# Optimization experiments

Measured on AMD Instinct MI355X. Metric: run time of the kernel, lower is better.

## Reference

```python
import jax, jax.numpy as jnp
import numpy as np

B, D_INPUT, D_MODEL, MEM, HID, N_SYNCH, OUT_DIMS, ITERS = 128, 512, 2048, 25, 32, 256, 1000, 24
SYNC = N_SYNCH * (N_SYNCH + 1) // 2  # 32896


def setup_inputs() -> dict:
    key = jax.random.key(0)
    ks = jax.random.split(key, 12)
    inp = {
        'x': jax.random.normal(ks[0], (B, D_INPUT), jnp.float32),
        'syn_w': jax.random.normal(ks[1], (D_INPUT + D_MODEL, 2 * D_MODEL), jnp.float32) * 0.02,
        'syn_b': jnp.zeros((2 * D_MODEL,), jnp.float32),
        'ln_g': jnp.ones((D_MODEL,), jnp.float32),
        'ln_b': jnp.zeros((D_MODEL,), jnp.float32),
        'tp_w1': jax.random.normal(ks[2], (MEM, 2 * HID, D_MODEL), jnp.float32) * (1.0 / np.sqrt(MEM + 2 * HID)),
        'tp_b1': jnp.zeros((1, D_MODEL, 2 * HID), jnp.float32),
        'tp_w2': jax.random.normal(ks[3], (HID, 2, D_MODEL), jnp.float32) * (1.0 / np.sqrt(HID + 2)),
        'tp_b2': jnp.zeros((1, D_MODEL, 2), jnp.float32),
        'start_activated_state': jax.random.normal(ks[4], (D_MODEL,), jnp.float32) * (1.0 / np.sqrt(D_MODEL)),
        'start_trace': jax.random.normal(ks[5], (D_MODEL, MEM), jnp.float32) * (1.0 / np.sqrt(D_MODEL + MEM)),
        'decay_params_out': jax.random.uniform(ks[6], (SYNC,), jnp.float32),
        'out_w': jax.random.normal(ks[7], (SYNC, OUT_DIMS), jnp.float32) * 0.02,
        'out_b': jnp.zeros((OUT_DIMS,), jnp.float32),
        'idx_left': jax.random.randint(ks[8], (N_SYNCH,), 0, D_MODEL),
        'idx_right': jax.random.randint(ks[9], (N_SYNCH,), 0, D_MODEL),
        'iterations': ITERS,
    }
    return inp


def _glu(z):
    a, b = jnp.split(z, 2, axis=-1)
    return a * jax.nn.sigmoid(b)


def reference(x, syn_w, syn_b, ln_g, ln_b, tp_w1, tp_b1, tp_w2, tp_b2,
              start_activated_state, start_trace, decay_params_out, out_w, out_b,
              idx_left, idx_right, iterations):
    Bx = x.shape[0]
    D, M = start_trace.shape
    n_synch = idx_left.shape[0]
    iu, ju = np.triu_indices(n_synch)
    r = jnp.exp(-jnp.clip(decay_params_out, 0.0, 15.0))[None, :]  # (1, S)
    log_nc = np.log(out_b.shape[0]).astype(np.float32)

    def pairwise(act):  # act: (B, D) -> (B, S) upper-tri of outer product of selected neurons
        l = act[:, idx_left]
        rr = act[:, idx_right]
        outer = l[:, :, None] * rr[:, None, :]
        return outer[:, iu, ju]

    def trace_proc(trace):  # (B, D, M) -> (B, D) per-neuron MLP (NLM)
        h = _glu(jnp.einsum('BDM,MHD->BDH', trace, tp_w1) + tp_b1)
        o = _glu(jnp.einsum('BDH,HOD->BDO', h, tp_w2) + tp_b2)
        return o[..., 0]

    def layernorm(z):
        mu = jnp.mean(z, -1, keepdims=True)
        var = jnp.mean((z - mu) ** 2, -1, keepdims=True)
        return (z - mu) * jax.lax.rsqrt(var + 1e-5) * ln_g + ln_b

    act0 = jnp.broadcast_to(start_activated_state[None, :], (Bx, D))
    trace0 = jnp.broadcast_to(start_trace[None, :, :], (Bx, D, M))
    alpha0 = pairwise(act0)
    beta0 = jnp.ones_like(alpha0)

    def step(carry, _):
        trace, act, alpha, beta = carry
        pre = jnp.concatenate([x, act], axis=-1)
        state = layernorm(_glu(pre @ syn_w + syn_b))            # (B, D)
        trace = jnp.concatenate([trace[:, :, 1:], state[:, :, None]], axis=-1)
        act = trace_proc(trace)                                  # (B, D)
        pp = pairwise(act)
        alpha = r * alpha + pp
        beta = r * beta + 1.0
        sync = alpha / jnp.sqrt(beta)                            # (B, S)
        pred = sync @ out_w + out_b                              # (B, out)
        logp = jax.nn.log_softmax(pred, axis=-1)
        ne = -jnp.sum(jnp.exp(logp) * logp, axis=-1) / log_nc
        cert = jnp.stack([ne, 1.0 - ne], axis=-1)                # (B, 2)
        return (trace, act, alpha, beta), (pred, cert)

    _, (preds, certs) = jax.lax.scan(step, (trace0, act0, alpha0, beta0), None, length=iterations)
    predictions = jnp.moveaxis(preds, 0, -1)   # (B, out_dims, T)
    certainties = jnp.moveaxis(certs, 0, -1)   # (B, 2, T)
    return predictions, certainties
```

## Files before the change

### kernel.cpp

```cpp
#include <hip/hip_runtime.h>
#include <stdint.h>

#define BB      128
#define DIN     512
#define DMODEL  2048
#define MEMN    25
#define NSY     256
#define OUTD    1000
#define ITERS   24
#define SYNCN   32896
#define KPAD    33792
#define NPAD    1024
#define NSPLIT  32
#define KCH     1056
#define PREDTOT (BB*OUTD*ITERS)

typedef __attribute__((ext_vector_type(8))) short bf16x8;
typedef __attribute__((ext_vector_type(4))) float f32x4;

__device__ __forceinline__ unsigned short f2bf(float x){
    unsigned int u = __float_as_uint(x);
    u += 0x7fffu + ((u >> 16) & 1u);
    return (unsigned short)(u >> 16);
}
__device__ __forceinline__ float bf2f(unsigned short h){
    unsigned int u = ((unsigned int)h) << 16;
    return __uint_as_float(u);
}
__device__ __forceinline__ float sigm(float x){ return 1.f/(1.f + __expf(-x)); }

__device__ __forceinline__ void gload16(const unsigned short* g, unsigned short* l){
    __builtin_amdgcn_global_load_lds(
        (const __attribute__((address_space(1))) unsigned int*)(const void*)g,
        (__attribute__((address_space(3))) unsigned int*)(void*)l,
        16, 0, 0);
}

__device__ __forceinline__ void reduce_row(const float* __restrict__ part, const float* __restrict__ outb,
    float* __restrict__ dout, float* red, int b, int t, int tid){
    float v[4];
    float m = -1e30f;
#pragma unroll
    for (int q = 0; q < 4; ++q){
        int n = q*256 + tid;
        float s;
        if (n < OUTD){
            s = outb[n];
            for (int sk = 0; sk < NSPLIT; ++sk)
                s += part[(long)sk*(BB*NPAD) + (long)b*NPAD + n];
        } else s = -1e30f;
        v[q] = s;
        m = fmaxf(m, s);
    }
#pragma unroll
    for (int off = 32; off; off >>= 1) m = fmaxf(m, __shfl_down(m, off));
    int w = tid >> 6;
    if ((tid & 63) == 0) red[w] = m;
    __syncthreads();
    float M = fmaxf(fmaxf(red[0], red[1]), fmaxf(red[2], red[3]));
    __syncthreads();
    float z = 0.f, s2 = 0.f;
#pragma unroll
    for (int q = 0; q < 4; ++q){
        int n = q*256 + tid;
        if (n < OUTD){
            float e = __expf(v[q] - M);
            z += e; s2 += e*v[q];
        }
    }
#pragma unroll
    for (int off = 32; off; off >>= 1){
        z  += __shfl_down(z, off);
        s2 += __shfl_down(s2, off);
    }
    if ((tid & 63) == 0){ red[w] = z; red[4+w] = s2; }
    __syncthreads();
    if (tid == 0){
        float Z = red[0]+red[1]+red[2]+red[3];
        float S = red[4]+red[5]+red[6]+red[7];
        float logZ = M + __logf(Z);
        float ne = (logZ - S/Z) / 6.907755278982137f;
        dout[PREDTOT + b*48 + t] = ne;
        dout[PREDTOT + b*48 + 24 + t] = 1.f - ne;
    }
#pragma unroll
    for (int q = 0; q < 4; ++q){
        int n = q*256 + tid;
        if (n < OUTD) dout[(long)b*(OUTD*ITERS) + (long)n*ITERS + t] = v[q];
    }
}


__global__ __launch_bounds__(256) void init_trace_k(const float* __restrict__ st,
    unsigned short* __restrict__ trh, unsigned short* __restrict__ trl){
    const long N = (long)MEMN*DMODEL*BB;
    for (long i = (long)blockIdx.x*256 + threadIdx.x; i < N; i += (long)gridDim.x*256){
        int m = (int)(i / (DMODEL*BB));
        int rem = (int)(i % (DMODEL*BB));
        int d = rem >> 7;
        float v = st[d*MEMN + m];
        unsigned short h = f2bf(v);
        trh[i] = h;
        trl[i] = f2bf(v - bf2f(h));
    }
}

__global__ __launch_bounds__(256) void init_act_k(const float* __restrict__ sas, float* __restrict__ act){
    for (int i = blockIdx.x*256 + threadIdx.x; i < DMODEL*BB; i += gridDim.x*256)
        act[i] = sas[i >> 7];
}

__global__ __launch_bounds__(256) void init_alpha_k(const float* __restrict__ sas,
    const int* __restrict__ il, const int* __restrict__ ir, float* __restrict__ alpha){
    int i = blockIdx.x, tid = threadIdx.x;
    if (tid >= NSY - i) return;
    int j = i + tid;
    int k = i*(2*NSY - i + 1)/2 + tid;
    float a0 = sas[il[i]] * sas[ir[j]];
    for (int b = 0; b < BB; ++b) alpha[b*SYNCN + k] = a0;
}

__global__ __launch_bounds__(256) void init_rowmap_k(int* __restrict__ rowOf, int* __restrict__ rowstart){
    int i = blockIdx.x, tid = threadIdx.x;
    int start = i*(2*NSY - i + 1)/2;
    int len = NSY - i;
    if (tid == 0) rowstart[i] = start;
    for (int t = tid; t < len; t += 256) rowOf[start + t] = i;
}

__global__ __launch_bounds__(256) void transpose_f32_k(const float* __restrict__ in, float* __restrict__ out, int R, int C){
    __shared__ float S[64][65];
    int r0 = blockIdx.y*64, c0 = blockIdx.x*64;
    for (int i = threadIdx.x; i < 64*64; i += 256){
        int rr = i >> 6, cc = i & 63;
        int r = r0+rr, c = c0+cc;
        if (r < R && c < C) S[rr][cc] = in[(long)r*C + c];
    }
    __syncthreads();
    for (int i = threadIdx.x; i < 64*64; i += 256){
        int cc = i >> 6, rr = i & 63;
        int r = r0+rr, c = c0+cc;
        if (r < R && c < C) out[(long)c*R + r] = S[rr][cc];
    }
}

__global__ __launch_bounds__(256) void w1bf_prep_k(const float* __restrict__ w1t, unsigned short* __restrict__ w1bf){
    int d = blockIdx.x, tid = threadIdx.x;
    __shared__ float S[1600];
    for (int i = tid; i < 1600; i += 256) S[i] = w1t[(long)d*1600 + i];
    __syncthreads();
    for (int i = tid; i < 2048; i += 256){
        int h = i >> 5, m = i & 31;
        float v = (m < MEMN) ? S[m*64 + h] : 0.f;
        unsigned short hi = f2bf(v);
        unsigned short lo = f2bf(v - bf2f(hi));
        w1bf[(long)d*4096 + i]        = hi;
        w1bf[(long)d*4096 + 2048 + i] = lo;
    }
}

__global__ __launch_bounds__(256) void wbf_transpose_k(const float* __restrict__ w, unsigned short* __restrict__ wt){
    __shared__ float S[64][65];
    int k0 = blockIdx.x*64, n0 = blockIdx.y*64;
    int tid = threadIdx.x;
    if (k0 >= SYNCN){
        uint4 z = {0u,0u,0u,0u};
#pragma unroll
        for (int p = 0; p < 2; ++p){
            int i = tid + p*256;
            int nn = i >> 3, k8 = (i & 7)*8;
            *(uint4*)(wt + (long)(n0+nn)*KPAD + k0 + k8) = z;
        }
        return;
    }
    const long MAXI = (long)SYNCN*OUTD - 4;
#pragma unroll
    for (int p = 0; p < 4; ++p){
        int i = tid + p*256;
        int rr = i >> 4, c4 = (i & 15)*4;
        long idx = (long)(k0+rr)*OUTD + n0 + c4;
        if (idx > MAXI) idx = MAXI;
        float4 v = *(const float4*)(w + idx);
        S[rr][c4+0]=v.x; S[rr][c4+1]=v.y; S[rr][c4+2]=v.z; S[rr][c4+3]=v.w;
    }
    __syncthreads();
#pragma unroll
    for (int p = 0; p < 4; ++p){
        int i = tid + p*256;
        int nn = i >> 4, k4 = (i & 15)*4;
        ushort4 o;
        o.x = f2bf(S[k4+0][nn]); o.y = f2bf(S[k4+1][nn]);
        o.z = f2bf(S[k4+2][nn]); o.w = f2bf(S[k4+3][nn]);
        *(ushort4*)(wt + (long)(n0+nn)*KPAD + k0 + k4) = o;
    }
}

__global__ __launch_bounds__(256) void swt_convert_k(const float* __restrict__ w,
    unsigned short* __restrict__ th, unsigned short* __restrict__ tl){
    __shared__ float S[64][65];
    int k0 = blockIdx.x*64, n0 = blockIdx.y*64;
    int tid = threadIdx.x;
#pragma unroll
    for (int p = 0; p < 4; ++p){
        int i = tid + p*256;
        int rr = i >> 4, c4 = (i & 15)*4;
        float4 v = *(const float4*)(w + (long)(512 + k0 + rr)*4096 + n0 + c4);
        S[rr][c4+0]=v.x; S[rr][c4+1]=v.y; S[rr][c4+2]=v.z; S[rr][c4+3]=v.w;
    }
    __syncthreads();
#pragma unroll
    for (int p = 0; p < 4; ++p){
        int i = tid + p*256;
        int nn = i >> 4, k4 = (i & 15)*4;
        ushort4 oh, ol;
        float v0 = S[k4+0][nn], v1 = S[k4+1][nn], v2 = S[k4+2][nn], v3 = S[k4+3][nn];
        oh.x = f2bf(v0); oh.y = f2bf(v1); oh.z = f2bf(v2); oh.w = f2bf(v3);
        ol.x = f2bf(v0 - bf2f(oh.x)); ol.y = f2bf(v1 - bf2f(oh.y));
        ol.z = f2bf(v2 - bf2f(oh.z)); ol.w = f2bf(v3 - bf2f(oh.w));
        *(ushort4*)(th + (long)(n0+nn)*DMODEL + k0 + k4) = oh;
        *(ushort4*)(tl + (long)(n0+nn)*DMODEL + k0 + k4) = ol;
    }
}

__global__ __launch_bounds__(256) void act_convert_k(const float* __restrict__ act,
    unsigned short* __restrict__ th, unsigned short* __restrict__ tl){
    __shared__ float S[64][65];
    int d0 = blockIdx.x*64, b0 = blockIdx.y*64;
    int tid = threadIdx.x;
#pragma unroll
    for (int p = 0; p < 4; ++p){
        int i = tid + p*256;
        int rr = i >> 4, c4 = (i & 15)*4;
        float4 v = *(const float4*)(act + (long)(d0+rr)*BB + b0 + c4);
        S[rr][c4+0]=v.x; S[rr][c4+1]=v.y; S[rr][c4+2]=v.z; S[rr][c4+3]=v.w;
    }
    __syncthreads();
#pragma unroll
    for (int p = 0; p < 4; ++p){
        int i = tid + p*256;
        int nn = i >> 4, k4 = (i & 15)*4;
        unsigned short h[4], l[4];
#pragma unroll
        for (int q = 0; q < 4; ++q){
            float v = S[k4+q][nn];
            h[q] = f2bf(v);
            l[q] = f2bf(v - bf2f(h[q]));
        }
        *(ushort4*)(th + (long)(b0+nn)*DMODEL + d0 + k4) = ushort4{h[0],h[1],h[2],h[3]};
        *(ushort4*)(tl + (long)(b0+nn)*DMODEL + d0 + k4) = ushort4{l[0],l[1],l[2],l[3]};
    }
}

__global__ __launch_bounds__(256) void gemm_syn_k(const float* __restrict__ A, const float* __restrict__ Bw,
    const float* __restrict__ bias, float* __restrict__ out){
    int j_base = blockIdx.x*64;
    int tid = threadIdx.x;
    __shared__ float As[16][128];
    __shared__ float Bs[16][68];
    int bg = tid & 15, jg = tid >> 4;
    int b0 = bg*8, j0 = jg*4;
    float acc[8][4];
#pragma unroll
    for (int i = 0; i < 8; ++i)
#pragma unroll
        for (int q = 0; q < 4; ++q) acc[i][q] = 0.f;
    for (int kt = 0; kt < 32; ++kt){
        {
            int i0 = tid*8;
            int kk = i0 >> 7, bb = i0 & 127;
            const float4* src = (const float4*)(A + (long)(kt*16+kk)*BB + bb);
            float4 v0 = src[0], v1 = src[1];
            *(float4*)&As[kk][bb]   = v0;
            *(float4*)&As[kk][bb+4] = v1;
        }
        {
            int i0 = tid*4;
            int kk = i0 >> 6, jj = i0 & 63;
            float4 v = *(const float4*)(Bw + (long)(kt*16+kk)*4096 + j_base + jj);
            *(float4*)&Bs[kk][jj] = v;
        }
        __syncthreads();
#pragma unroll
        for (int kk = 0; kk < 16; ++kk){
            float a[8], bv[4];
            *(float4*)&a[0] = *(float4*)&As[kk][b0];
            *(float4*)&a[4] = *(float4*)&As[kk][b0+4];
            *(float4*)&bv[0] = *(float4*)&Bs[kk][j0];
#pragma unroll
            for (int i = 0; i < 8; ++i)
#pragma unroll
                for (int q = 0; q < 4; ++q) acc[i][q] += a[i]*bv[q];
        }
        __syncthreads();
    }
#pragma unroll
    for (int i = 0; i < 8; ++i){
        int bb = b0 + i;
        float4 v;
        v.x = acc[i][0]+bias[j_base+j0+0]; v.y = acc[i][1]+bias[j_base+j0+1];
        v.z = acc[i][2]+bias[j_base+j0+2]; v.w = acc[i][3]+bias[j_base+j0+3];
        *(float4*)(out + (long)bb*4096 + j_base + j0) = v;
    }
}


__global__ __launch_bounds__(256) void syn_mfma_k(const unsigned short* __restrict__ Ah, const unsigned short* __restrict__ Al,
    const unsigned short* __restrict__ Bh, const unsigned short* __restrict__ Bl, float* __restrict__ zpart,
    const float* __restrict__ part, const float* __restrict__ outb, float* __restrict__ dout, int tprev){
    __shared__ __align__(16) unsigned short As_h[128*32], As_l[128*32], Bs_h[64*32], Bs_l[64*32];
    __shared__ float red[8];
    int tid = threadIdx.x;

    if (blockIdx.y == 8){
        if (tprev >= 0){
            reduce_row(part, outb, dout, red, 2*blockIdx.x,   tprev, tid);
            __syncthreads();
            reduce_row(part, outb, dout, red, 2*blockIdx.x+1, tprev, tid);
        }
        return;
    }

    int nb = blockIdx.x;
    int s  = blockIdx.y;
    int wid = tid >> 6, lane = tid & 63;
    int wm = (wid & 1)*64, wn = (wid >> 1)*32;

    f32x4 c[4][2];
#pragma unroll
    for (int a = 0; a < 4; ++a)
#pragma unroll
        for (int b = 0; b < 2; ++b) c[a][b] = (f32x4){0.f,0.f,0.f,0.f};

    int mrow = lane & 15, kq = lane >> 4;
    int srow = tid >> 2;
    int ksg  = (tid & 3)*8;
    long koff0 = (long)s*256 + ksg;
    const unsigned short* gAh1 = Ah + (long)srow*DMODEL      + koff0;
    const unsigned short* gAh2 = Ah + (long)(srow+64)*DMODEL + koff0;
    const unsigned short* gAl1 = Al + (long)srow*DMODEL      + koff0;
    const unsigned short* gAl2 = Al + (long)(srow+64)*DMODEL + koff0;
    const unsigned short* gBh  = Bh + (long)(nb*64+srow)*DMODEL + koff0;
    const unsigned short* gBl  = Bl + (long)(nb*64+srow)*DMODEL + koff0;
    unsigned short* lAh1 = As_h + wid*512;
    unsigned short* lAh2 = As_h + 2048 + wid*512;
    unsigned short* lAl1 = As_l + wid*512;
    unsigned short* lAl2 = As_l + 2048 + wid*512;
    unsigned short* lBh  = Bs_h + wid*512;
    unsigned short* lBl  = Bs_l + wid*512;

    for (int ks = 0; ks < 8; ++ks){
        int o = ks*32;
        gload16(gAh1 + o, lAh1);
        gload16(gAh2 + o, lAh2);
        gload16(gAl1 + o, lAl1);
        gload16(gAl2 + o, lAl2);
        gload16(gBh  + o, lBh);
        gload16(gBl  + o, lBl);
        __syncthreads();
        bf16x8 ah[4], al[4], bh[2], bl[2];
#pragma unroll
        for (int x = 0; x < 4; ++x){
            ah[x] = *(const bf16x8*)&As_h[(wm + x*16 + mrow)*32 + kq*8];
            al[x] = *(const bf16x8*)&As_l[(wm + x*16 + mrow)*32 + kq*8];
        }
#pragma unroll
        for (int y = 0; y < 2; ++y){
            bh[y] = *(const bf16x8*)&Bs_h[(wn + y*16 + mrow)*32 + kq*8];
            bl[y] = *(const bf16x8*)&Bs_l[(wn + y*16 + mrow)*32 + kq*8];
        }
#pragma unroll
        for (int a = 0; a < 4; ++a)
#pragma unroll
            for (int b = 0; b < 2; ++b){
                c[a][b] = __builtin_amdgcn_mfma_f32_16x16x32_bf16(ah[a], bh[b], c[a][b], 0, 0, 0);
                c[a][b] = __builtin_amdgcn_mfma_f32_16x16x32_bf16(al[a], bh[b], c[a][b], 0, 0, 0);
                c[a][b] = __builtin_amdgcn_mfma_f32_16x16x32_bf16(ah[a], bl[b], c[a][b], 0, 0, 0);
            }
        __syncthreads();
    }
    float* outp = zpart + (long)s*(BB*4096);
#pragma unroll
    for (int a = 0; a < 4; ++a)
#pragma unroll
        for (int b = 0; b < 2; ++b){
            int r0 = wm + a*16 + (lane >> 4)*4;
            int col = nb*64 + wn + b*16 + (lane & 15);
#pragma unroll
            for (int reg = 0; reg < 4; ++reg)
                outp[(long)(r0+reg)*4096 + col] = c[a][b][reg];
        }
}

__global__ __launch_bounds__(1024) void glu_ln_k(const float* __restrict__ C0, const float* __restrict__ zp,
    const float* __restrict__ lng, const float* __restrict__ lnb,
    unsigned short* __restrict__ trh, unsigned short* __restrict__ trl, int slot){
    int b = blockIdx.x, tid = threadIdx.x;
    __shared__ float redA[16], redB[16];
    int d0 = tid*2;
    const float* base = C0 + (long)b*4096;
    float2 a = *(const float2*)(base + d0);
    float2 g = *(const float2*)(base + 2048 + d0);
#pragma unroll
    for (int s = 0; s < 8; ++s){
        const float* zb = zp + (long)s*524288 + (long)b*4096;
        float2 az = *(const float2*)(zb + d0);
        float2 gz = *(const float2*)(zb + 2048 + d0);
        a.x += az.x; a.y += az.y; g.x += gz.x; g.y += gz.y;
    }
    float v0 = a.x*sigm(g.x), v1 = a.y*sigm(g.y);
    float s1 = v0+v1, s2 = v0*v0+v1*v1;
#pragma unroll
    for (int off = 32; off; off >>= 1){
        s1 += __shfl_down(s1, off);
        s2 += __shfl_down(s2, off);
    }
    if ((tid & 63) == 0){ redA[tid>>6] = s1; redB[tid>>6] = s2; }
    __syncthreads();
    if (tid == 0){
        float sa = 0.f, sb = 0.f;
        for (int i = 0; i < 16; ++i){ sa += redA[i]; sb += redB[i]; }
        float mu = sa*(1.f/2048.f);
        float var = sb*(1.f/2048.f) - mu*mu;
        redA[0] = mu;
        redB[0] = rsqrtf(var + 1e-5f);
    }
    __syncthreads();
    float mu = redA[0], inv = redB[0];
    float st0 = (v0-mu)*inv*lng[d0]   + lnb[d0];
    float st1 = (v1-mu)*inv*lng[d0+1] + lnb[d0+1];
    unsigned short h0 = f2bf(st0), h1 = f2bf(st1);
    long o0 = ((long)slot*DMODEL + d0)*BB + b;
    trh[o0]      = h0;  trl[o0]      = f2bf(st0 - bf2f(h0));
    trh[o0 + BB] = h1;  trl[o0 + BB] = f2bf(st1 - bf2f(h1));
}

__global__ __launch_bounds__(256) void trace_proc_k(
    const unsigned short* __restrict__ trh, const unsigned short* __restrict__ trl,
    const unsigned short* __restrict__ w1bf,
    const float* __restrict__ b1, const float* __restrict__ w2t, const float* __restrict__ b2,
    float* __restrict__ act, unsigned short* __restrict__ aTh, unsigned short* __restrict__ aTl, int t){
    int d = blockIdx.x, tid = threadIdx.x;
    __shared__ __align__(16) unsigned short Ah[128*40];
    __shared__ __align__(16) unsigned short Al[128*40];
    __shared__ __align__(16) unsigned short Bbuf[4096];
    __shared__ float hh[128*33];
    __shared__ float w2s[64];

    for (int i = tid; i < MEMN*64; i += 256){
        int m = i >> 6, bp = i & 63;
        int phys = t + 1 + m; if (phys >= MEMN) phys -= MEMN; if (phys >= MEMN) phys -= MEMN;
        long gaddr = ((long)phys*DMODEL + d)*BB + bp*2;
        ushort2 vh = *(const ushort2*)(trh + gaddr);
        ushort2 vl = *(const ushort2*)(trl + gaddr);
        Ah[(bp*2+0)*40 + m] = vh.x; Ah[(bp*2+1)*40 + m] = vh.y;
        Al[(bp*2+0)*40 + m] = vl.x; Al[(bp*2+1)*40 + m] = vl.y;
    }
    for (int i = tid; i < 7*128; i += 256){
        int m = MEMN + (i >> 7), b = i & 127;
        Ah[b*40 + m] = 0; Al[b*40 + m] = 0;
    }
    {
        const uint4* src = (const uint4*)(w1bf + (long)d*4096);
        uint4* dst = (uint4*)Bbuf;
        for (int i = tid; i < 512; i += 256) dst[i] = src[i];
    }
    if (tid < 64) w2s[tid] = w2t[(long)d*64 + tid];
    __syncthreads();

    int wid = tid >> 6, lane = tid & 63;
    int mrow = lane & 15, kq = lane >> 4;
    bf16x8 ahf[2], alf[2], bhf[4], blf[4];
#pragma unroll
    for (int bt = 0; bt < 2; ++bt){
        int r = (wid*2 + bt)*16 + mrow;
        ahf[bt] = *(const bf16x8*)&Ah[r*40 + kq*8];
        alf[bt] = *(const bf16x8*)&Al[r*40 + kq*8];
    }
#pragma unroll
    for (int ht = 0; ht < 4; ++ht){
        int r = ht*16 + mrow;
        bhf[ht] = *(const bf16x8*)&Bbuf[r*32 + kq*8];
        blf[ht] = *(const bf16x8*)&Bbuf[2048 + r*32 + kq*8];
    }
    f32x4 c[2][4];
#pragma unroll
    for (int bt = 0; bt < 2; ++bt)
#pragma unroll
        for (int ht = 0; ht < 4; ++ht){
            c[bt][ht] = (f32x4){0.f,0.f,0.f,0.f};
            c[bt][ht] = __builtin_amdgcn_mfma_f32_16x16x32_bf16(ahf[bt], bhf[ht], c[bt][ht], 0, 0, 0);
            c[bt][ht] = __builtin_amdgcn_mfma_f32_16x16x32_bf16(alf[bt], bhf[ht], c[bt][ht], 0, 0, 0);
            c[bt][ht] = __builtin_amdgcn_mfma_f32_16x16x32_bf16(ahf[bt], blf[ht], c[bt][ht], 0, 0, 0);
        }
    int quad = lane >> 4;
#pragma unroll
    for (int bt = 0; bt < 2; ++bt){
        int bb0 = (wid*2 + bt)*16 + quad*4;
#pragma unroll
        for (int ht = 0; ht < 2; ++ht){
            int h = ht*16 + (lane & 15);
            float ba = b1[(long)d*64 + h];
            float bg = b1[(long)d*64 + 32 + h];
#pragma unroll
            for (int reg = 0; reg < 4; ++reg){
                float a = c[bt][ht][reg] + ba;
                float g = c[bt][ht+2][reg] + bg;
                hh[(bb0+reg)*33 + h] = a * sigm(g);
            }
        }
    }
    __syncthreads();
    if (tid < 128){
        int bb = tid;
        float o0 = b2[(long)d*2+0], o1 = b2[(long)d*2+1];
#pragma unroll
        for (int h = 0; h < 32; ++h){
            float hv = hh[bb*33 + h];
            o0 += hv * w2s[h*2+0];
            o1 += hv * w2s[h*2+1];
        }
        float a = o0 * sigm(o1);
        act[(long)d*BB + bb] = a;
        unsigned short h16 = f2bf(a);
        aTh[(long)bb*DMODEL + d] = h16;
        aTl[(long)bb*DMODEL + d] = f2bf(a - bf2f(h16));
    }
}

__global__ __launch_bounds__(256) void pairwise_sync_k(const float* __restrict__ act, const float* __restrict__ decay,
    const int* __restrict__ il, const int* __restrict__ ir,
    const int* __restrict__ rowOf, const int* __restrict__ rowstart,
    float* __restrict__ alpha, unsigned short* __restrict__ syncb, int t){
    int k = blockIdx.x*256 + threadIdx.x;
    int bg = blockIdx.y;
    int blo = bg*32, bhi = blo + 32;
    if (k >= SYNCN){
        if (k < KPAD)
            for (int b = blo; b < bhi; ++b) syncb[(long)b*KPAD + k] = 0;
        return;
    }
    int i = rowOf[k];
    int j = i + (k - rowstart[i]);
    float cc = fminf(fmaxf(decay[k], 0.f), 15.f);
    float r = __expf(-cc);
    float bet;
    if (cc < 1e-30f) bet = (float)(t + 2);
    else {
        float e1 = expm1f(-cc);
        float et = expm1f(-cc*(float)(t+1));
        bet = 1.f + et + et/e1;
    }
    float rs = rsqrtf(bet);
    const float* aL = act + (long)il[i]*BB;
    const float* aR = act + (long)ir[j]*BB;
    for (int b = blo; b < bhi; ++b){
        float pp = aL[b]*aR[b];
        float al = r*alpha[(long)b*SYNCN + k] + pp;
        alpha[(long)b*SYNCN + k] = al;
        syncb[(long)b*KPAD + k] = f2bf(al*rs);
    }
}

__global__ __launch_bounds__(256) void out_gemm_k(const unsigned short* __restrict__ Abf,
    const unsigned short* __restrict__ Bbf, float* __restrict__ part){
    int n_base = blockIdx.x*64;
    int sk = blockIdx.y;
    int tid = threadIdx.x;
    int wid = tid >> 6, lane = tid & 63;
    int wm = (wid & 1)*64, wn = (wid >> 1)*32;
    long k_base = (long)sk*KCH;
    __shared__ __align__(16) unsigned short As[128*32];
    __shared__ __align__(16) unsigned short Bs[64*32];
    f32x4 c[4][2];
#pragma unroll
    for (int a = 0; a < 4; ++a)
#pragma unroll
        for (int b = 0; b < 2; ++b) c[a][b] = (f32x4){0.f,0.f,0.f,0.f};

    int mrow = lane & 15, kq = lane >> 4;
    int srow = tid >> 2;
    int ksg  = (tid & 3)*8;
    const unsigned short* gA1 = Abf + (long)srow*KPAD      + k_base + ksg;
    const unsigned short* gA2 = Abf + (long)(srow+64)*KPAD + k_base + ksg;
    const unsigned short* gB  = Bbf + (long)(n_base+srow)*KPAD + k_base + ksg;
    unsigned short* lA1 = As + wid*512;
    unsigned short* lA2 = As + 2048 + wid*512;
    unsigned short* lB  = Bs + wid*512;

    for (int ks = 0; ks < KCH/32; ++ks){
        int o = ks*32;
        gload16(gA1 + o, lA1);
        gload16(gA2 + o, lA2);
        gload16(gB  + o, lB);
        __syncthreads();
        bf16x8 af[4], bf[2];
#pragma unroll
        for (int x = 0; x < 4; ++x)
            af[x] = *(const bf16x8*)&As[(wm + x*16 + mrow)*32 + kq*8];
#pragma unroll
        for (int y = 0; y < 2; ++y)
            bf[y] = *(const bf16x8*)&Bs[(wn + y*16 + mrow)*32 + kq*8];
#pragma unroll
        for (int a = 0; a < 4; ++a)
#pragma unroll
            for (int b = 0; b < 2; ++b)
                c[a][b] = __builtin_amdgcn_mfma_f32_16x16x32_bf16(af[a], bf[b], c[a][b], 0, 0, 0);
        __syncthreads();
    }
    float* outp = part + (long)sk*(128*NPAD);
#pragma unroll
    for (int a = 0; a < 4; ++a)
#pragma unroll
        for (int b = 0; b < 2; ++b){
            int r0 = wm + a*16 + (lane >> 4)*4;
            int col = n_base + wn + b*16 + (lane & 15);
#pragma unroll
            for (int reg = 0; reg < 4; ++reg)
                outp[(long)(r0+reg)*NPAD + col] = c[a][b][reg];
        }
}

__global__ __launch_bounds__(256) void reduce_final_k(const float* __restrict__ part,
    const float* __restrict__ outb, float* __restrict__ dout){
    __shared__ float red[8];
    reduce_row(part, outb, dout, red, blockIdx.x, ITERS-1, threadIdx.x);
}


extern "C" void kernel_launch(void* const* d_in, const int* in_sizes, int n_in,
                              void* d_out, int out_size, void* d_ws, size_t ws_size,
                              hipStream_t stream){
    const float* x      = (const float*)d_in[0];
    const float* syn_w  = (const float*)d_in[1];
    const float* syn_b  = (const float*)d_in[2];
    const float* ln_g   = (const float*)d_in[3];
    const float* ln_b   = (const float*)d_in[4];
    const float* tp_w1  = (const float*)d_in[5];
    const float* tp_b1  = (const float*)d_in[6];
    const float* tp_w2  = (const float*)d_in[7];
    const float* tp_b2  = (const float*)d_in[8];
    const float* sas    = (const float*)d_in[9];
    const float* strc   = (const float*)d_in[10];
    const float* decay  = (const float*)d_in[11];
    const float* out_w  = (const float*)d_in[12];
    const float* out_b  = (const float*)d_in[13];
    const int*   il     = (const int*)d_in[14];
    const int*   ir     = (const int*)d_in[15];
    float* dout = (float*)d_out;

    char* ws = (char*)d_ws;
    size_t off = 0;
    auto alloc = [&](size_t bytes)->void*{
        void* p = ws + off;
        off += (bytes + 255) & ~(size_t)255;
        return p;
    };
    unsigned short* trh = (unsigned short*)alloc((size_t)MEMN*DMODEL*BB*2);
    unsigned short* trl = (unsigned short*)alloc((size_t)MEMN*DMODEL*BB*2);
    float* act     = (float*)alloc((size_t)DMODEL*BB*4);
    float* C0      = (float*)alloc((size_t)BB*4096*4);
    float* xt      = (float*)alloc((size_t)DIN*BB*4);
    float* w2t     = (float*)alloc((size_t)DMODEL*64*4);
    unsigned short* w1bf = (unsigned short*)alloc((size_t)DMODEL*4096*2);
    float* alpha   = (float*)alloc((size_t)BB*SYNCN*4);
    unsigned short* syncb = (unsigned short*)alloc((size_t)BB*KPAD*2);
    unsigned short* wbt   = (unsigned short*)alloc((size_t)NPAD*KPAD*2);
    float* part    = (float*)alloc((size_t)NSPLIT*BB*NPAD*4);
    float* w1t     = part;
    float* zpart   = (float*)alloc((size_t)8*BB*4096*4);
    unsigned short* swT_h = (unsigned short*)alloc((size_t)4096*DMODEL*2);
    unsigned short* swT_l = (unsigned short*)alloc((size_t)4096*DMODEL*2);
    unsigned short* aT_h  = (unsigned short*)alloc((size_t)BB*DMODEL*2);
    unsigned short* aT_l  = (unsigned short*)alloc((size_t)BB*DMODEL*2);
    int* rowOf    = (int*)alloc((size_t)SYNCN*4);
    int* rowstart = (int*)alloc((size_t)NSY*4);
    (void)ws_size; (void)in_sizes; (void)n_in; (void)out_size;

    init_trace_k<<<8192, 256, 0, stream>>>(strc, trh, trl);
    init_act_k<<<1024, 256, 0, stream>>>(sas, act);
    init_alpha_k<<<256, 256, 0, stream>>>(sas, il, ir, alpha);
    init_rowmap_k<<<256, 256, 0, stream>>>(rowOf, rowstart);
    transpose_f32_k<<<dim3(32, 25), 256, 0, stream>>>(tp_w1, w1t, 1600, 2048);
    w1bf_prep_k<<<2048, 256, 0, stream>>>(w1t, w1bf);
    transpose_f32_k<<<dim3(32, 1),  256, 0, stream>>>(tp_w2, w2t, 64, 2048);
    transpose_f32_k<<<dim3(8, 2),   256, 0, stream>>>(x, xt, 128, 512);
    wbf_transpose_k<<<dim3(KPAD/64, 16), 256, 0, stream>>>(out_w, wbt);
    swt_convert_k<<<dim3(32, 64), 256, 0, stream>>>(syn_w, swT_h, swT_l);
    gemm_syn_k<<<64, 256, 0, stream>>>(xt, syn_w, syn_b, C0);
    act_convert_k<<<dim3(32, 2), 256, 0, stream>>>(act, aT_h, aT_l);

    for (int t = 0; t < ITERS; ++t){
        syn_mfma_k<<<dim3(64, 9), 256, 0, stream>>>(aT_h, aT_l, swT_h, swT_l, zpart,
                                                    part, out_b, dout, t - 1);
        glu_ln_k<<<128, 1024, 0, stream>>>(C0, zpart, ln_g, ln_b, trh, trl, t % MEMN);
        trace_proc_k<<<2048, 256, 0, stream>>>(trh, trl, w1bf, tp_b1, w2t, tp_b2, act, aT_h, aT_l, t);
        pairwise_sync_k<<<dim3(KPAD/256, 4), 256, 0, stream>>>(act, decay, il, ir, rowOf, rowstart, alpha, syncb, t);
        out_gemm_k<<<dim3(16, NSPLIT), 256, 0, stream>>>(syncb, wbt, part);
    }
    reduce_final_k<<<128, 256, 0, stream>>>(part, out_b, dout);
}
```

Baseline: 2.779 ms.

## Overlap output GEMM of previous step with next step's synapse GEMM

Delays the output projection GEMM for step t-1 so it runs as extra blocks inside the same launch as the synapse MFMA GEMM of step t, since the two are independent. The softmax/certainty reduction for step t-1 moves into the GLU/layernorm launch as extra blocks, and the last step's output GEMM runs after the loop. This removes one launch per iteration and fills the GPU with more concurrent blocks, at the cost of a larger unified kernel with shared LDS sizing and more complex scheduling.

After: 2.582 ms. 1.08x faster.

```diff
diff --git a/kernel.cpp b/kernel.cpp
--- a/kernel.cpp
+++ b/kernel.cpp
@@ -304,134 +304,233 @@
 }
 
 
-__global__ __launch_bounds__(256) void syn_mfma_k(const unsigned short* __restrict__ Ah, const unsigned short* __restrict__ Al,
-    const unsigned short* __restrict__ Bh, const unsigned short* __restrict__ Bl, float* __restrict__ zpart,
-    const float* __restrict__ part, const float* __restrict__ outb, float* __restrict__ dout, int tprev){
-    __shared__ __align__(16) unsigned short As_h[128*32], As_l[128*32], Bs_h[64*32], Bs_l[64*32];
-    __shared__ float red[8];
+__global__ __launch_bounds__(256) void mfma_pair_k(
+    const unsigned short* __restrict__ Ah, const unsigned short* __restrict__ Al,
+    const unsigned short* __restrict__ Bh, const unsigned short* __restrict__ Bl,
+    float* __restrict__ zpart,
+    const unsigned short* __restrict__ Abf, const unsigned short* __restrict__ Bbf,
+    float* __restrict__ part, int has_out){
+    __shared__ __align__(16) unsigned short smem[12288];
     int tid = threadIdx.x;
-
-    if (blockIdx.y == 8){
-        if (tprev >= 0){
-            reduce_row(part, outb, dout, red, 2*blockIdx.x,   tprev, tid);
-            __syncthreads();
-            reduce_row(part, outb, dout, red, 2*blockIdx.x+1, tprev, tid);
-        }
-        return;
-    }
-
-    int nb = blockIdx.x;
-    int s  = blockIdx.y;
+    int bid = blockIdx.x;
     int wid = tid >> 6, lane = tid & 63;
     int wm = (wid & 1)*64, wn = (wid >> 1)*32;
-
-    f32x4 c[4][2];
-#pragma unroll
-    for (int a = 0; a < 4; ++a)
-#pragma unroll
-        for (int b = 0; b < 2; ++b) c[a][b] = (f32x4){0.f,0.f,0.f,0.f};
-
     int mrow = lane & 15, kq = lane >> 4;
     int srow = tid >> 2;
     int ksg  = (tid & 3)*8;
-    long koff0 = (long)s*256 + ksg;
-    const unsigned short* gAh1 = Ah + (long)srow*DMODEL      + koff0;
-    const unsigned short* gAh2 = Ah + (long)(srow+64)*DMODEL + koff0;
-    const unsigned short* gAl1 = Al + (long)srow*DMODEL      + koff0;
-    const unsigned short* gAl2 = Al + (long)(srow+64)*DMODEL + koff0;
-    const unsigned short* gBh  = Bh + (long)(nb*64+srow)*DMODEL + koff0;
-    const unsigned short* gBl  = Bl + (long)(nb*64+srow)*DMODEL + koff0;
-    unsigned short* lAh1 = As_h + wid*512;
-    unsigned short* lAh2 = As_h + 2048 + wid*512;
-    unsigned short* lAl1 = As_l + wid*512;
-    unsigned short* lAl2 = As_l + 2048 + wid*512;
-    unsigned short* lBh  = Bs_h + wid*512;
-    unsigned short* lBl  = Bs_l + wid*512;
-
-    for (int ks = 0; ks < 8; ++ks){
-        int o = ks*32;
-        gload16(gAh1 + o, lAh1);
-        gload16(gAh2 + o, lAh2);
-        gload16(gAl1 + o, lAl1);
-        gload16(gAl2 + o, lAl2);
-        gload16(gBh  + o, lBh);
-        gload16(gBl  + o, lBl);
-        __syncthreads();
-        bf16x8 ah[4], al[4], bh[2], bl[2];
-#pragma unroll
-        for (int x = 0; x < 4; ++x){
-            ah[x] = *(const bf16x8*)&As_h[(wm + x*16 + mrow)*32 + kq*8];
-            al[x] = *(const bf16x8*)&As_l[(wm + x*16 + mrow)*32 + kq*8];
-        }
-#pragma unroll
-        for (int y = 0; y < 2; ++y){
-            bh[y] = *(const bf16x8*)&Bs_h[(wn + y*16 + mrow)*32 + kq*8];
-            bl[y] = *(const bf16x8*)&Bs_l[(wn + y*16 + mrow)*32 + kq*8];
-        }
+
+    if (bid < 512){
+        unsigned short* As_h = smem;
+        unsigned short* As_l = smem + 4096;
+        unsigned short* Bs_h = smem + 8192;
+        unsigned short* Bs_l = smem + 10240;
+        int nb = bid & 63;
+        int s  = bid >> 6;
+
+        f32x4 c[4][2];
 #pragma unroll
         for (int a = 0; a < 4; ++a)
 #pragma unroll
+            for (int b = 0; b < 2; ++b) c[a][b] = (f32x4){0.f,0.f,0.f,0.f};
+
+        long koff0 = (long)s*256 + ksg;
+        const unsigned short* gAh1 = Ah + (long)srow*DMODEL      + koff0;
+        const unsigned short* gAh2 = Ah + (long)(srow+64)*DMODEL + koff0;
+        const unsigned short* gAl1 = Al + (long)srow*DMODEL      + koff0;
+        const unsigned short* gAl2 = Al + (long)(srow+64)*DMODEL + koff0;
+        const unsigned short* gBh  = Bh + (long)(nb*64+srow)*DMODEL + koff0;
+        const unsigned short* gBl  = Bl + (long)(nb*64+srow)*DMODEL + koff0;
+        unsigned short* lAh1 = As_h + wid*512;
+        unsigned short* lAh2 = As_h + 2048 + wid*512;
+        unsigned short* lAl1 = As_l + wid*512;
+        unsigned short* lAl2 = As_l + 2048 + wid*512;
+        unsigned short* lBh  = Bs_h + wid*512;
+        unsigned short* lBl  = Bs_l + wid*512;
+
+        for (int ks = 0; ks < 8; ++ks){
+            int o = ks*32;
+            gload16(gAh1 + o, lAh1);
+            gload16(gAh2 + o, lAh2);
+            gload16(gAl1 + o, lAl1);
+            gload16(gAl2 + o, lAl2);
+            gload16(gBh  + o, lBh);
+            gload16(gBl  + o, lBl);
+            __syncthreads();
+            bf16x8 ah[4], al[4], bh[2], bl[2];
+#pragma unroll
+            for (int x = 0; x < 4; ++x){
+                ah[x] = *(const bf16x8*)&As_h[(wm + x*16 + mrow)*32 + kq*8];
+                al[x] = *(const bf16x8*)&As_l[(wm + x*16 + mrow)*32 + kq*8];
+            }
+#pragma unroll
+            for (int y = 0; y < 2; ++y){
+                bh[y] = *(const bf16x8*)&Bs_h[(wn + y*16 + mrow)*32 + kq*8];
+                bl[y] = *(const bf16x8*)&Bs_l[(wn + y*16 + mrow)*32 + kq*8];
+            }
+#pragma unroll
+            for (int a = 0; a < 4; ++a)
+#pragma unroll
+                for (int b = 0; b < 2; ++b){
+                    c[a][b] = __builtin_amdgcn_mfma_f32_16x16x32_bf16(ah[a], bh[b], c[a][b], 0, 0, 0);
+                    c[a][b] = __builtin_amdgcn_mfma_f32_16x16x32_bf16(al[a], bh[b], c[a][b], 0, 0, 0);
+                    c[a][b] = __builtin_amdgcn_mfma_f32_16x16x32_bf16(ah[a], bl[b], c[a][b], 0, 0, 0);
+                }
+            __syncthreads();
+        }
+        float* outp = zpart + (long)s*(BB*4096);
+#pragma unroll
+        for (int a = 0; a < 4; ++a)
+#pragma unroll
             for (int b = 0; b < 2; ++b){
-                c[a][b] = __builtin_amdgcn_mfma_f32_16x16x32_bf16(ah[a], bh[b], c[a][b], 0, 0, 0);
-                c[a][b] = __builtin_amdgcn_mfma_f32_16x16x32_bf16(al[a], bh[b], c[a][b], 0, 0, 0);
-                c[a][b] = __builtin_amdgcn_mfma_f32_16x16x32_bf16(ah[a], bl[b], c[a][b], 0, 0, 0);
+                int r0 = wm + a*16 + (lane >> 4)*4;
+                int col = nb*64 + wn + b*16 + (lane & 15);
+#pragma unroll
+                for (int reg = 0; reg < 4; ++reg)
+                    outp[(long)(r0+reg)*4096 + col] = c[a][b][reg];
             }
-        __syncthreads();
-    }
-    float* outp = zpart + (long)s*(BB*4096);
-#pragma unroll
-    for (int a = 0; a < 4; ++a)
-#pragma unroll
-        for (int b = 0; b < 2; ++b){
-            int r0 = wm + a*16 + (lane >> 4)*4;
-            int col = nb*64 + wn + b*16 + (lane & 15);
-#pragma unroll
-            for (int reg = 0; reg < 4; ++reg)
-                outp[(long)(r0+reg)*4096 + col] = c[a][b][reg];
-        }
-}
-
-__global__ __launch_bounds__(1024) void glu_ln_k(const float* __restrict__ C0, const float* __restrict__ zp,
+    } else {
+        if (!has_out) return;
+        unsigned short* As = smem;
+        unsigned short* Bs = smem + 4096;
+        int idx = bid - 512;
+        int sk = idx >> 4;
+        int n_base = (idx & 15)*64;
+        long k_base = (long)sk*KCH;
+
+        f32x4 c[4][2];
+#pragma unroll
+        for (int a = 0; a < 4; ++a)
+#pragma unroll
+            for (int b = 0; b < 2; ++b) c[a][b] = (f32x4){0.f,0.f,0.f,0.f};
+
+        const unsigned short* gA1 = Abf + (long)srow*KPAD      + k_base + ksg;
+        const unsigned short* gA2 = Abf + (long)(srow+64)*KPAD + k_base + ksg;
+        const unsigned short* gB  = Bbf + (long)(n_base+srow)*KPAD + k_base + ksg;
+        unsigned short* lA1 = As + wid*512;
+        unsigned short* lA2 = As + 2048 + wid*512;
+        unsigned short* lB  = Bs + wid*512;
+
+        for (int ks = 0; ks < KCH/32; ++ks){
+            int o = ks*32;
+            gload16(gA1 + o, lA1);
+            gload16(gA2 + o, lA2);
+            gload16(gB  + o, lB);
+            __syncthreads();
+            bf16x8 af[4], bf[2];
+#pragma unroll
+            for (int x = 0; x < 4; ++x)
+                af[x] = *(const bf16x8*)&As[(wm + x*16 + mrow)*32 + kq*8];
+#pragma unroll
+            for (int y = 0; y < 2; ++y)
+                bf[y] = *(const bf16x8*)&Bs[(wn + y*16 + mrow)*32 + kq*8];
+#pragma unroll
+            for (int a = 0; a < 4; ++a)
+#pragma unroll
+                for (int b = 0; b < 2; ++b)
+                    c[a][b] = __builtin_amdgcn_mfma_f32_16x16x32_bf16(af[a], bf[b], c[a][b], 0, 0, 0);
+            __syncthreads();
+        }
+        float* outp = part + (long)sk*(128*NPAD);
+#pragma unroll
+        for (int a = 0; a < 4; ++a)
+#pragma unroll
+            for (int b = 0; b < 2; ++b){
+                int r0 = wm + a*16 + (lane >> 4)*4;
+                int col = n_base + wn + b*16 + (lane & 15);
+#pragma unroll
+                for (int reg = 0; reg < 4; ++reg)
+                    outp[(long)(r0+reg)*NPAD + col] = c[a][b][reg];
+            }
+    }
+}
+
+__global__ __launch_bounds__(1024) void glu_red_k(const float* __restrict__ C0, const float* __restrict__ zp,
     const float* __restrict__ lng, const float* __restrict__ lnb,
-    unsigned short* __restrict__ trh, unsigned short* __restrict__ trl, int slot){
-    int b = blockIdx.x, tid = threadIdx.x;
+    unsigned short* __restrict__ trh, unsigned short* __restrict__ trl, int slot,
+    const float* __restrict__ part, const float* __restrict__ outb, float* __restrict__ dout, int tprev){
     __shared__ float redA[16], redB[16];
-    int d0 = tid*2;
-    const float* base = C0 + (long)b*4096;
-    float2 a = *(const float2*)(base + d0);
-    float2 g = *(const float2*)(base + 2048 + d0);
-#pragma unroll
-    for (int s = 0; s < 8; ++s){
-        const float* zb = zp + (long)s*524288 + (long)b*4096;
-        float2 az = *(const float2*)(zb + d0);
-        float2 gz = *(const float2*)(zb + 2048 + d0);
-        a.x += az.x; a.y += az.y; g.x += gz.x; g.y += gz.y;
-    }
-    float v0 = a.x*sigm(g.x), v1 = a.y*sigm(g.y);
-    float s1 = v0+v1, s2 = v0*v0+v1*v1;
-#pragma unroll
-    for (int off = 32; off; off >>= 1){
-        s1 += __shfl_down(s1, off);
-        s2 += __shfl_down(s2, off);
-    }
-    if ((tid & 63) == 0){ redA[tid>>6] = s1; redB[tid>>6] = s2; }
-    __syncthreads();
-    if (tid == 0){
-        float sa = 0.f, sb = 0.f;
-        for (int i = 0; i < 16; ++i){ sa += redA[i]; sb += redB[i]; }
-        float mu = sa*(1.f/2048.f);
-        float var = sb*(1.f/2048.f) - mu*mu;
-        redA[0] = mu;
-        redB[0] = rsqrtf(var + 1e-5f);
-    }
-    __syncthreads();
-    float mu = redA[0], inv = redB[0];
-    float st0 = (v0-mu)*inv*lng[d0]   + lnb[d0];
-    float st1 = (v1-mu)*inv*lng[d0+1] + lnb[d0+1];
-    unsigned short h0 = f2bf(st0), h1 = f2bf(st1);
-    long o0 = ((long)slot*DMODEL + d0)*BB + b;
-    trh[o0]      = h0;  trl[o0]      = f2bf(st0 - bf2f(h0));
-    trh[o0 + BB] = h1;  trl[o0 + BB] = f2bf(st1 - bf2f(h1));
+    int tid = threadIdx.x;
+    if (blockIdx.x < 128){
+        int b = blockIdx.x;
+        int d0 = tid*2;
+        const float* base = C0 + (long)b*4096;
+        float2 a = *(const float2*)(base + d0);
+        float2 g = *(const float2*)(base + 2048 + d0);
+#pragma unroll
+        for (int s = 0; s < 8; ++s){
+            const float* zb = zp + (long)s*524288 + (long)b*4096;
+            float2 az = *(const float2*)(zb + d0);
+            float2 gz = *(const float2*)(zb + 2048 + d0);
+            a.x += az.x; a.y += az.y; g.x += gz.x; g.y += gz.y;
+        }
+        float v0 = a.x*sigm(g.x), v1 = a.y*sigm(g.y);
+        float s1 = v0+v1, s2 = v0*v0+v1*v1;
+#pragma unroll
+        for (int off = 32; off; off >>= 1){
+            s1 += __shfl_down(s1, off);
+            s2 += __shfl_down(s2, off);
+        }
+        if ((tid & 63) == 0){ redA[tid>>6] = s1; redB[tid>>6] = s2; }
+        __syncthreads();
+        if (tid == 0){
+            float sa = 0.f, sb = 0.f;
+            for (int i = 0; i < 16; ++i){ sa += redA[i]; sb += redB[i]; }
+            float mu = sa*(1.f/2048.f);
+            float var = sb*(1.f/2048.f) - mu*mu;
+            redA[0] = mu;
+            redB[0] = rsqrtf(var + 1e-5f);
+        }
+        __syncthreads();
+        float mu = redA[0], inv = redB[0];
+        float st0 = (v0-mu)*inv*lng[d0]   + lnb[d0];
+        float st1 = (v1-mu)*inv*lng[d0+1] + lnb[d0+1];
+        unsigned short h0 = f2bf(st0), h1 = f2bf(st1);
+        long o0 = ((long)slot*DMODEL + d0)*BB + b;
+        trh[o0]      = h0;  trl[o0]      = f2bf(st0 - bf2f(h0));
+        trh[o0 + BB] = h1;  trl[o0 + BB] = f2bf(st1 - bf2f(h1));
+    } else {
+        if (tprev < 0) return;
+        int b = blockIdx.x - 128;
+        float v = -1e30f;
+        if (tid < OUTD){
+            float s = outb[tid];
+            for (int sk = 0; sk < NSPLIT; ++sk)
+                s += part[(long)sk*(BB*NPAD) + (long)b*NPAD + tid];
+            v = s;
+        }
+        float m = v;
+#pragma unroll
+        for (int off = 32; off; off >>= 1) m = fmaxf(m, __shfl_down(m, off));
+        if ((tid & 63) == 0) redA[tid>>6] = m;
+        __syncthreads();
+        if (tid == 0){
+            float r = redA[0];
+            for (int i = 1; i < 16; ++i) r = fmaxf(r, redA[i]);
+            redA[0] = r;
+        }
+        __syncthreads();
+        float M = redA[0];
+        __syncthreads();
+        float e  = (tid < OUTD) ? __expf(v - M) : 0.f;
+        float ev = e * ((tid < OUTD) ? v : 0.f);
+        float z = e, s2 = ev;
+#pragma unroll
+        for (int off = 32; off; off >>= 1){
+            z  += __shfl_down(z, off);
+            s2 += __shfl_down(s2, off);
+        }
+        if ((tid & 63) == 0){ redA[tid>>6] = z; redB[tid>>6] = s2; }
+        __syncthreads();
+        if (tid == 0){
+            float Z = 0.f, S = 0.f;
+            for (int i = 0; i < 16; ++i){ Z += redA[i]; S += redB[i]; }
+            float logZ = M + __logf(Z);
+            float ne = (logZ - S/Z) / 6.907755278982137f;
+            dout[PREDTOT + b*48 + tprev] = ne;
+            dout[PREDTOT + b*48 + 24 + tprev] = 1.f - ne;
+        }
+        if (tid < OUTD) dout[(long)b*(OUTD*ITERS) + (long)tid*ITERS + tprev] = v;
+    }
 }
 
 __global__ __launch_bounds__(256) void trace_proc_k(
@@ -690,12 +789,13 @@
     act_convert_k<<<dim3(32, 2), 256, 0, stream>>>(act, aT_h, aT_l);
 
     for (int t = 0; t < ITERS; ++t){
-        syn_mfma_k<<<dim3(64, 9), 256, 0, stream>>>(aT_h, aT_l, swT_h, swT_l, zpart,
-                                                    part, out_b, dout, t - 1);
-        glu_ln_k<<<128, 1024, 0, stream>>>(C0, zpart, ln_g, ln_b, trh, trl, t % MEMN);
+        mfma_pair_k<<<1024, 256, 0, stream>>>(aT_h, aT_l, swT_h, swT_l, zpart,
+                                              syncb, wbt, part, t > 0);
+        glu_red_k<<<256, 1024, 0, stream>>>(C0, zpart, ln_g, ln_b, trh, trl, t % MEMN,
+                                            part, out_b, dout, t - 1);
         trace_proc_k<<<2048, 256, 0, stream>>>(trh, trl, w1bf, tp_b1, w2t, tp_b2, act, aT_h, aT_l, t);
         pairwise_sync_k<<<dim3(KPAD/256, 4), 256, 0, stream>>>(act, decay, il, ir, rowOf, rowstart, alpha, syncb, t);
-        out_gemm_k<<<dim3(16, NSPLIT), 256, 0, stream>>>(syncb, wbt, part);
-    }
+    }
+    out_gemm_k<<<dim3(16, NSPLIT), 256, 0, stream>>>(syncb, wbt, part);
     reduce_final_k<<<128, 256, 0, stream>>>(part, out_b, dout);
 }
```
